# Kernel tuning notes

Measured on AMD Instinct MI355X. Metric: run time of the kernel, lower is better.

Reference implementation:

```python
import jax, jax.numpy as jnp
import numpy as np

EMBED_DIMS = 1024
NUM_HEADS = 16
HEAD_DIMS = EMBED_DIMS // NUM_HEADS


def setup_inputs() -> dict:
    key = jax.random.key(0)
    k_x, k_wqkv, k_bqkv, k_wp, k_bp = jax.random.split(key, 5)
    B, N, D = 2, 2048, EMBED_DIMS
    x = jax.random.normal(k_x, (B, N, D), dtype=jnp.float32)
    # torch nn.Linear(in, out): weight [out, in], y = x @ W.T + b
    s = 1.0 / np.sqrt(D)
    W_qkv = jax.random.uniform(k_wqkv, (3 * D, D), jnp.float32, -s, s)
    b_qkv = jax.random.uniform(k_bqkv, (3 * D,), jnp.float32, -s, s)
    W_proj = jax.random.uniform(k_wp, (D, D), jnp.float32, -s, s)
    b_proj = jax.random.uniform(k_bp, (D,), jnp.float32, -s, s)
    return {"x": x, "W_qkv": W_qkv, "b_qkv": b_qkv, "W_proj": W_proj, "b_proj": b_proj}


def reference(x, W_qkv, b_qkv, W_proj, b_proj):
    B, N, D = x.shape
    H, Hd = NUM_HEADS, HEAD_DIMS
    # qkv projection: [B, N, 3, H, Hd] -> split q, k, v as [B, H, N, Hd]
    qkv = (x @ W_qkv.T + b_qkv).reshape(B, N, 3, H, Hd).transpose(2, 0, 3, 1, 4)
    q, k, v = qkv[0], qkv[1], qkv[2]
    scale = 1.0 / jnp.sqrt(jnp.asarray(Hd, x.dtype))
    attn = jnp.einsum("bhqd,bhkd->bhqk", q, k) * scale  # [B, H, N, N]
    attn = jax.nn.softmax(attn, axis=-1)
    out = jnp.einsum("bhqk,bhkd->bhqd", attn, v)  # [B, H, N, Hd]
    out = out.transpose(0, 2, 1, 3).reshape(B, N, D)
    out = out @ W_proj.T + b_proj
    return out
```

## Files before the change

kernel.cpp:

```cpp
#include <hip/hip_runtime.h>

typedef _Float16 f16x8 __attribute__((ext_vector_type(8)));
typedef __attribute__((ext_vector_type(4))) float f32x4;

static __device__ __forceinline__ unsigned short f2h(float f) {
  return __builtin_bit_cast(unsigned short, (_Float16)f);
}

static __device__ __forceinline__ unsigned int pk2(float a, float b) {
  return (unsigned int)f2h(a) | ((unsigned int)f2h(b) << 16);
}

#if __has_builtin(__builtin_amdgcn_cvt_pkrtz)
static __device__ __forceinline__ unsigned int pkrtz(float a, float b) {
  return __builtin_bit_cast(unsigned int, __builtin_amdgcn_cvt_pkrtz(a, b));
}
#else
#define pkrtz pk2
#endif

#if __has_builtin(__builtin_amdgcn_exp2f)
#define EXP2(x) __builtin_amdgcn_exp2f(x)
#else
#define EXP2(x) exp2f(x)
#endif

#define GLOAD_LDS16(gp, lp)                                          \
  __builtin_amdgcn_global_load_lds(                                  \
      (const __attribute__((address_space(1))) unsigned int*)(gp),   \
      (__attribute__((address_space(3))) unsigned int*)(lp), 16, 0, 0)

__global__ __launch_bounds__(256) void cvt_all(
    const float* __restrict__ X, const float* __restrict__ Wq,
    const float* __restrict__ Wp, unsigned short* __restrict__ Xb,
    unsigned short* __restrict__ Wqb, unsigned short* __restrict__ Wpb) {
  const int i = blockIdx.x * 256 + threadIdx.x;
  const float4* src;
  unsigned short* dst;
  int off;
  if (i < 1048576) {
    src = (const float4*)X; dst = Xb; off = i;
  } else if (i < 1835008) {
    src = (const float4*)Wq; dst = Wqb; off = i - 1048576;
  } else {
    src = (const float4*)Wp; dst = Wpb; off = i - 1835008;
  }
  const float4 v = src[off];
  *(ushort4*)(dst + (size_t)off * 4) =
      make_ushort4(f2h(v.x), f2h(v.y), f2h(v.z), f2h(v.w));
}

__global__ __launch_bounds__(256, 3) void qkv_gemm(
    const unsigned short* __restrict__ Xb, const unsigned short* __restrict__ Wb,
    const float* __restrict__ bias, unsigned short* __restrict__ Qb,
    unsigned short* __restrict__ Kb, unsigned short* __restrict__ Vt) {
  __shared__ __align__(16) unsigned short A_sh[2][128 * 32];
  __shared__ __align__(16) unsigned short B_sh[2][128 * 32];
  const int n0 = blockIdx.x * 128, m0 = blockIdx.y * 128;
  const int tid = threadIdx.x, lane = tid & 63, wave = tid >> 6;
  const int wr = wave >> 1, wc = wave & 1;
  const int lm = lane & 15, lg = lane >> 4;
  const int r4 = lane >> 2;
  const int sg8 = (((lane & 3) ^ ((r4 >> 1) & 3)) * 8);
  const int lgx = (lg ^ ((lm >> 1) & 3)) * 8;

  f32x4 acc[4][4] = {};

#define QSTAGE(k0_, b_)                                                       \
  do {                                                                        \
    _Pragma("unroll")                                                         \
    for (int j = 0; j < 2; ++j) {                                             \
      const int chunk = wave * 2 + j;                                         \
      const int row = chunk * 16 + r4;                                        \
      GLOAD_LDS16(Xb + (size_t)(m0 + row) * 1024 + (k0_) + sg8,               \
                  &A_sh[b_][chunk * 512]);                                    \
      GLOAD_LDS16(Wb + (size_t)(n0 + row) * 1024 + (k0_) + sg8,               \
                  &B_sh[b_][chunk * 512]);                                    \
    }                                                                         \
  } while (0)

  QSTAGE(0, 0);

  for (int it = 0; it < 32; ++it) {
    const int cur = it & 1;
    __syncthreads();
    if (it < 31) QSTAGE((it + 1) * 32, cur ^ 1);

    f16x8 af[4], bfr[4];
#pragma unroll
    for (int mi = 0; mi < 4; ++mi)
      af[mi] = *(const f16x8*)&A_sh[cur][(wr * 64 + mi * 16 + lm) * 32 + lgx];
#pragma unroll
    for (int ni = 0; ni < 4; ++ni)
      bfr[ni] = *(const f16x8*)&B_sh[cur][(wc * 64 + ni * 16 + lm) * 32 + lgx];
    __builtin_amdgcn_s_setprio(1);
#pragma unroll
    for (int mi = 0; mi < 4; ++mi)
#pragma unroll
      for (int ni = 0; ni < 4; ++ni)
        acc[mi][ni] = __builtin_amdgcn_mfma_f32_16x16x32_f16(
            af[mi], bfr[ni], acc[mi][ni], 0, 0, 0);
    __builtin_amdgcn_s_setprio(0);
  }
#undef QSTAGE

  const float qscale = 0.18033688011112042f;
#pragma unroll
  for (int mi = 0; mi < 4; ++mi) {
#pragma unroll
    for (int ni = 0; ni < 4; ++ni) {
      const int gn = n0 + wc * 64 + ni * 16 + lm;
      const float bv = bias[gn];
      const int which = gn >> 10;
      const int h = (gn >> 6) & 15;
      const int hd = gn & 63;
      float v[4];
#pragma unroll
      for (int r = 0; r < 4; ++r) v[r] = acc[mi][ni][r] + bv;
      const int gm0 = m0 + wr * 64 + mi * 16 + lg * 4;
      const int bb = gm0 >> 11;
      const int nq0 = gm0 & 2047;
      if (which == 0) {
        unsigned short* p = Qb + (((size_t)bb * 16 + h) * 2048 + nq0) * 64 + hd;
        p[0] = f2h(v[0] * qscale);   p[64] = f2h(v[1] * qscale);
        p[128] = f2h(v[2] * qscale); p[192] = f2h(v[3] * qscale);
      } else if (which == 1) {
        unsigned short* p = Kb + (((size_t)bb * 16 + h) * 2048 + nq0) * 64 + hd;
        p[0] = f2h(v[0]);   p[64] = f2h(v[1]);
        p[128] = f2h(v[2]); p[192] = f2h(v[3]);
      } else {
        *(ushort4*)(Vt + (((size_t)bb * 16 + h) * 64 + hd) * 2048 + nq0) =
            make_ushort4(f2h(v[0]), f2h(v[1]), f2h(v[2]), f2h(v[3]));
      }
    }
  }
}

__global__ __launch_bounds__(1024, 4) void attn_kernel(
    const unsigned short* __restrict__ Qb, const unsigned short* __restrict__ Kb,
    const unsigned short* __restrict__ Vt, unsigned short* __restrict__ Ob) {
  __shared__ __align__(16) unsigned short K_sh[2][2][64 * 32];
  __shared__ __align__(16) unsigned short V_sh[2][2][64 * 32];
  __shared__ __align__(16) f32x4 Om[8][5][64];
  const int bh = blockIdx.y, q0 = blockIdx.x * 256;
  const size_t base = (size_t)bh * (2048 * 64);
  const unsigned short* Qp = Qb + base;
  const unsigned short* Kp = Kb + base;
  const unsigned short* Vp = Vt + base;
  const int tid = threadIdx.x, lane = tid & 63, wave = tid >> 6;
  const int lm = lane & 15, lg = lane >> 4;
  const int r4 = lane >> 2;
  const int sg8 = (((lane & 3) ^ ((r4 >> 1) & 3)) * 8);
  const int lgx = (lg ^ ((lm >> 1) & 3)) * 8;

  const int qg = wave >> 1;
  const int khalf = wave & 1;

  f16x8 vones;
#pragma unroll
  for (int j = 0; j < 8; ++j) vones[j] = (_Float16)1.0f;

  f16x8 qf[2][2];
#pragma unroll
  for (int mi = 0; mi < 2; ++mi)
#pragma unroll
    for (int kc = 0; kc < 2; ++kc)
      qf[mi][kc] = *(const f16x8*)(Qp +
          (size_t)(q0 + qg * 32 + mi * 16 + lm) * 64 + kc * 32 + lg * 8);

  f32x4 o[2][4] = {};
  f32x4 o_ones[2] = {};

  const bool isV = wave >= 8;
  const int sw = wave & 7;
  const int plane = sw & 1;
  const int chunk = sw >> 1;

#define STAGE(kt_, b_)                                                        \
  do {                                                                        \
    if (!isV) {                                                               \
      GLOAD_LDS16(Kp + (size_t)((kt_) * 64 + chunk * 16 + r4) * 64 +          \
                      plane * 32 + sg8,                                       \
                  &K_sh[b_][plane][chunk * 512]);                             \
    } else {                                                                  \
      GLOAD_LDS16(Vp + (size_t)(chunk * 16 + r4) * 2048 +                     \
                      (kt_) * 64 + plane * 32 + sg8,                          \
                  &V_sh[b_][plane][chunk * 512]);                             \
    }                                                                         \
  } while (0)

  STAGE(0, 0);

  for (int kt = 0; kt < 32; ++kt) {
    const int cur = kt & 1;
    __syncthreads();
    if (kt < 31) STAGE(kt + 1, cur ^ 1);

    f32x4 s[2][2] = {};
#pragma unroll
    for (int kc = 0; kc < 2; ++kc) {
#pragma unroll
      for (int ni = 0; ni < 2; ++ni) {
        const f16x8 kf = *(const f16x8*)
            &K_sh[cur][kc][(khalf * 32 + ni * 16 + lm) * 32 + lgx];
        __builtin_amdgcn_s_setprio(1);
        s[0][ni] = __builtin_amdgcn_mfma_f32_16x16x32_f16(
            kf, qf[0][kc], s[0][ni], 0, 0, 0);
        s[1][ni] = __builtin_amdgcn_mfma_f32_16x16x32_f16(
            kf, qf[1][kc], s[1][ni], 0, 0, 0);
        __builtin_amdgcn_s_setprio(0);
      }
    }

    unsigned int Wp_[2][2][2];
#pragma unroll
    for (int mi = 0; mi < 2; ++mi)
#pragma unroll
      for (int ni = 0; ni < 2; ++ni) {
        const float p0 = EXP2(s[mi][ni][0]), p1 = EXP2(s[mi][ni][1]);
        const float p2 = EXP2(s[mi][ni][2]), p3 = EXP2(s[mi][ni][3]);
        Wp_[mi][ni][0] = pkrtz(p0, p1);
        Wp_[mi][ni][1] = pkrtz(p2, p3);
      }

    f16x8 vb[4];
#pragma unroll
    for (int ni = 0; ni < 4; ++ni)
      vb[ni] = *(const f16x8*)&V_sh[cur][khalf][(ni * 16 + lm) * 32 + lgx];

#pragma unroll
    for (int mi = 0; mi < 2; ++mi) {
      auto t0 = __builtin_amdgcn_permlane32_swap(Wp_[mi][0][0], Wp_[mi][1][0],
                                                 false, false);
      auto u0 = __builtin_amdgcn_permlane16_swap(t0[0], t0[1], false, false);
      auto t1 = __builtin_amdgcn_permlane32_swap(Wp_[mi][0][1], Wp_[mi][1][1],
                                                 false, false);
      auto u1 = __builtin_amdgcn_permlane16_swap(t1[0], t1[1], false, false);
      union { unsigned int u[4]; f16x8 v; } pa;
      pa.u[0] = u0[0];
      pa.u[1] = u1[0];
      pa.u[2] = u0[1];
      pa.u[3] = u1[1];
      __builtin_amdgcn_s_setprio(1);
#pragma unroll
      for (int ni = 0; ni < 4; ++ni)
        o[mi][ni] = __builtin_amdgcn_mfma_f32_16x16x32_f16(
            pa.v, vb[ni], o[mi][ni], 0, 0, 0);
      o_ones[mi] = __builtin_amdgcn_mfma_f32_16x16x32_f16(
          pa.v, vones, o_ones[mi], 0, 0, 0);
      __builtin_amdgcn_s_setprio(0);
    }
  }
#undef STAGE

  const int b = bh >> 4, h = bh & 15;
#pragma unroll
  for (int mi = 0; mi < 2; ++mi) {
    __syncthreads();
    if (khalf == 1) {
#pragma unroll
      for (int ni = 0; ni < 4; ++ni) Om[qg][ni][lane] = o[mi][ni];
      Om[qg][4][lane] = o_ones[mi];
    }
    __syncthreads();
    if (khalf == 0) {
#pragma unroll
      for (int ni = 0; ni < 4; ++ni) {
        const f32x4 t = Om[qg][ni][lane];
        o[mi][ni][0] += t[0]; o[mi][ni][1] += t[1];
        o[mi][ni][2] += t[2]; o[mi][ni][3] += t[3];
      }
      const f32x4 t4 = Om[qg][4][lane];
#pragma unroll
      for (int r = 0; r < 4; ++r) {
        const float inv = 1.0f / (o_ones[mi][r] + t4[r]);
        const int nq = q0 + qg * 32 + mi * 16 + lg * 4 + r;
        unsigned short* p = Ob + ((size_t)(b * 2048 + nq) * 16 + h) * 64 + lm;
        p[0] = f2h(o[mi][0][r] * inv);
        p[16] = f2h(o[mi][1][r] * inv);
        p[32] = f2h(o[mi][2][r] * inv);
        p[48] = f2h(o[mi][3][r] * inv);
      }
    }
  }
}

__global__ __launch_bounds__(256) void proj_gemm(
    const unsigned short* __restrict__ A, const unsigned short* __restrict__ Wb,
    const float* __restrict__ bias, float* __restrict__ Out) {
  __shared__ __align__(16) unsigned short A_sh[2][64 * 32];
  __shared__ __align__(16) unsigned short B_sh[2][128 * 32];
  const int n0 = blockIdx.x * 128, m0 = blockIdx.y * 64;
  const int tid = threadIdx.x, lane = tid & 63, wave = tid >> 6;
  const int wr = wave >> 1, wc = wave & 1, lm = lane & 15, lg = lane >> 4;
  const int r4 = lane >> 2;
  const int sg8 = (((lane & 3) ^ ((r4 >> 1) & 3)) * 8);
  const int lgx = (lg ^ ((lm >> 1) & 3)) * 8;

  f32x4 acc[2][4] = {};

#define PSTAGE(k0_, b_)                                                       \
  do {                                                                        \
    {                                                                         \
      const int row = wave * 16 + r4;                                         \
      GLOAD_LDS16(A + (size_t)(m0 + row) * 1024 + (k0_) + sg8,                \
                  &A_sh[b_][wave * 512]);                                     \
    }                                                                         \
    _Pragma("unroll")                                                         \
    for (int j = 0; j < 2; ++j) {                                             \
      const int chunk = wave * 2 + j;                                         \
      const int row = chunk * 16 + r4;                                        \
      GLOAD_LDS16(Wb + (size_t)(n0 + row) * 1024 + (k0_) + sg8,               \
                  &B_sh[b_][chunk * 512]);                                    \
    }                                                                         \
  } while (0)

  PSTAGE(0, 0);

  for (int it = 0; it < 32; ++it) {
    const int cur = it & 1;
    __syncthreads();
    if (it < 31) PSTAGE((it + 1) * 32, cur ^ 1);

    f16x8 af[2], bfr[4];
#pragma unroll
    for (int mi = 0; mi < 2; ++mi)
      af[mi] = *(const f16x8*)&A_sh[cur][(wr * 32 + mi * 16 + lm) * 32 + lgx];
#pragma unroll
    for (int ni = 0; ni < 4; ++ni)
      bfr[ni] = *(const f16x8*)&B_sh[cur][(wc * 64 + ni * 16 + lm) * 32 + lgx];
#pragma unroll
    for (int mi = 0; mi < 2; ++mi)
#pragma unroll
      for (int ni = 0; ni < 4; ++ni)
        acc[mi][ni] = __builtin_amdgcn_mfma_f32_16x16x32_f16(
            af[mi], bfr[ni], acc[mi][ni], 0, 0, 0);
  }
#undef PSTAGE

#pragma unroll
  for (int mi = 0; mi < 2; ++mi)
#pragma unroll
    for (int ni = 0; ni < 4; ++ni) {
      const int gn = n0 + wc * 64 + ni * 16 + lm;
      const float bv = bias[gn];
#pragma unroll
      for (int r = 0; r < 4; ++r) {
        const int gm = m0 + wr * 32 + mi * 16 + lg * 4 + r;
        Out[(size_t)gm * 1024 + gn] = acc[mi][ni][r] + bv;
      }
    }
}

extern "C" void kernel_launch(void* const* d_in, const int* in_sizes, int n_in,
                              void* d_out, int out_size, void* d_ws, size_t ws_size,
                              hipStream_t stream) {
  const float* x      = (const float*)d_in[0];
  const float* W_qkv  = (const float*)d_in[1];
  const float* b_qkv  = (const float*)d_in[2];
  const float* W_proj = (const float*)d_in[3];
  const float* b_proj = (const float*)d_in[4];
  float* out = (float*)d_out;

  unsigned short* Qb  = (unsigned short*)d_ws;
  unsigned short* Kb  = Qb + 4194304;
  unsigned short* Vt  = Kb + 4194304;
  unsigned short* Ao  = Vt + 4194304;
  unsigned short* Xb  = Ao + 4194304;
  unsigned short* Wqb = Xb + 4194304;
  unsigned short* Wpb = Wqb + 3145728;

  cvt_all<<<8192, 256, 0, stream>>>(x, W_qkv, W_proj, Xb, Wqb, Wpb);
  qkv_gemm<<<dim3(24, 32), 256, 0, stream>>>(Xb, Wqb, b_qkv, Qb, Kb, Vt);
  attn_kernel<<<dim3(8, 32), 1024, 0, stream>>>(Qb, Kb, Vt, Ao);
  proj_gemm<<<dim3(8, 64), 256, 0, stream>>>(Ao, Wpb, b_proj, out);
}
```

Measured before the change: 182.1 us.

## Stage two KV tiles per barrier in attention and raise GEMM occupancy bounds

The attention kernel now loads two 64-key tiles per pipeline stage into doubled LDS buffers, so there is one __syncthreads per 128 keys instead of per 64. The QK MFMA priority bump now wraps the whole score loop rather than each pair. The qkv and proj GEMMs also get a min-blocks-per-CU of 4 in launch_bounds, which pushes register use down. In exchange, attention LDS use roughly doubles for K/V, which may lower occupancy, and the tighter register limits on the GEMMs could cause spills.

After: 179.2 us. Within noise of the previous version (-1.6%).

```diff
diff --git a/kernel.cpp b/kernel.cpp
--- a/kernel.cpp
+++ b/kernel.cpp
@@ -50,7 +50,7 @@
       make_ushort4(f2h(v.x), f2h(v.y), f2h(v.z), f2h(v.w));
 }
 
-__global__ __launch_bounds__(256, 3) void qkv_gemm(
+__global__ __launch_bounds__(256, 4) void qkv_gemm(
     const unsigned short* __restrict__ Xb, const unsigned short* __restrict__ Wb,
     const float* __restrict__ bias, unsigned short* __restrict__ Qb,
     unsigned short* __restrict__ Kb, unsigned short* __restrict__ Vt) {
@@ -139,8 +139,8 @@
 __global__ __launch_bounds__(1024, 4) void attn_kernel(
     const unsigned short* __restrict__ Qb, const unsigned short* __restrict__ Kb,
     const unsigned short* __restrict__ Vt, unsigned short* __restrict__ Ob) {
-  __shared__ __align__(16) unsigned short K_sh[2][2][64 * 32];
-  __shared__ __align__(16) unsigned short V_sh[2][2][64 * 32];
+  __shared__ __align__(16) unsigned short K_sh[2][2][2][64 * 32];
+  __shared__ __align__(16) unsigned short V_sh[2][2][2][64 * 32];
   __shared__ __align__(16) f32x4 Om[8][5][64];
   const int bh = blockIdx.y, q0 = blockIdx.x * 256;
   const size_t base = (size_t)bh * (2048 * 64);
@@ -176,82 +176,91 @@
   const int plane = sw & 1;
   const int chunk = sw >> 1;
 
-#define STAGE(kt_, b_)                                                        \
+#define STAGE1(kt_, b_, t_)                                                   \
   do {                                                                        \
     if (!isV) {                                                               \
       GLOAD_LDS16(Kp + (size_t)((kt_) * 64 + chunk * 16 + r4) * 64 +          \
                       plane * 32 + sg8,                                       \
-                  &K_sh[b_][plane][chunk * 512]);                             \
+                  &K_sh[b_][t_][plane][chunk * 512]);                         \
     } else {                                                                  \
       GLOAD_LDS16(Vp + (size_t)(chunk * 16 + r4) * 2048 +                     \
                       (kt_) * 64 + plane * 32 + sg8,                          \
-                  &V_sh[b_][plane][chunk * 512]);                             \
+                  &V_sh[b_][t_][plane][chunk * 512]);                         \
     }                                                                         \
   } while (0)
 
-  STAGE(0, 0);
-
-  for (int kt = 0; kt < 32; ++kt) {
-    const int cur = kt & 1;
-    __syncthreads();
-    if (kt < 31) STAGE(kt + 1, cur ^ 1);
-
-    f32x4 s[2][2] = {};
-#pragma unroll
-    for (int kc = 0; kc < 2; ++kc) {
-#pragma unroll
-      for (int ni = 0; ni < 2; ++ni) {
-        const f16x8 kf = *(const f16x8*)
-            &K_sh[cur][kc][(khalf * 32 + ni * 16 + lm) * 32 + lgx];
-        __builtin_amdgcn_s_setprio(1);
-        s[0][ni] = __builtin_amdgcn_mfma_f32_16x16x32_f16(
-            kf, qf[0][kc], s[0][ni], 0, 0, 0);
-        s[1][ni] = __builtin_amdgcn_mfma_f32_16x16x32_f16(
-            kf, qf[1][kc], s[1][ni], 0, 0, 0);
-        __builtin_amdgcn_s_setprio(0);
-      }
-    }
-
-    unsigned int Wp_[2][2][2];
-#pragma unroll
-    for (int mi = 0; mi < 2; ++mi)
-#pragma unroll
-      for (int ni = 0; ni < 2; ++ni) {
-        const float p0 = EXP2(s[mi][ni][0]), p1 = EXP2(s[mi][ni][1]);
-        const float p2 = EXP2(s[mi][ni][2]), p3 = EXP2(s[mi][ni][3]);
-        Wp_[mi][ni][0] = pkrtz(p0, p1);
-        Wp_[mi][ni][1] = pkrtz(p2, p3);
-      }
-
-    f16x8 vb[4];
-#pragma unroll
-    for (int ni = 0; ni < 4; ++ni)
-      vb[ni] = *(const f16x8*)&V_sh[cur][khalf][(ni * 16 + lm) * 32 + lgx];
-
-#pragma unroll
-    for (int mi = 0; mi < 2; ++mi) {
-      auto t0 = __builtin_amdgcn_permlane32_swap(Wp_[mi][0][0], Wp_[mi][1][0],
-                                                 false, false);
-      auto u0 = __builtin_amdgcn_permlane16_swap(t0[0], t0[1], false, false);
-      auto t1 = __builtin_amdgcn_permlane32_swap(Wp_[mi][0][1], Wp_[mi][1][1],
-                                                 false, false);
-      auto u1 = __builtin_amdgcn_permlane16_swap(t1[0], t1[1], false, false);
-      union { unsigned int u[4]; f16x8 v; } pa;
-      pa.u[0] = u0[0];
-      pa.u[1] = u1[0];
-      pa.u[2] = u0[1];
-      pa.u[3] = u1[1];
-      __builtin_amdgcn_s_setprio(1);
-#pragma unroll
-      for (int ni = 0; ni < 4; ++ni)
-        o[mi][ni] = __builtin_amdgcn_mfma_f32_16x16x32_f16(
-            pa.v, vb[ni], o[mi][ni], 0, 0, 0);
-      o_ones[mi] = __builtin_amdgcn_mfma_f32_16x16x32_f16(
-          pa.v, vones, o_ones[mi], 0, 0, 0);
-      __builtin_amdgcn_s_setprio(0);
-    }
-  }
-#undef STAGE
+#define STAGE2(seg_, b_)                                                      \
+  do { STAGE1(2 * (seg_), b_, 0); STAGE1(2 * (seg_) + 1, b_, 1); } while (0)
+
+#define TILE_COMPUTE(cur_, t_)                                                \
+  do {                                                                        \
+    f32x4 s[2][2] = {};                                                       \
+    __builtin_amdgcn_s_setprio(1);                                            \
+    _Pragma("unroll")                                                         \
+    for (int kc = 0; kc < 2; ++kc) {                                          \
+      _Pragma("unroll")                                                       \
+      for (int ni = 0; ni < 2; ++ni) {                                        \
+        const f16x8 kf = *(const f16x8*)                                      \
+            &K_sh[cur_][t_][kc][(khalf * 32 + ni * 16 + lm) * 32 + lgx];      \
+        s[0][ni] = __builtin_amdgcn_mfma_f32_16x16x32_f16(                    \
+            kf, qf[0][kc], s[0][ni], 0, 0, 0);                                \
+        s[1][ni] = __builtin_amdgcn_mfma_f32_16x16x32_f16(                    \
+            kf, qf[1][kc], s[1][ni], 0, 0, 0);                                \
+      }                                                                       \
+    }                                                                         \
+    __builtin_amdgcn_s_setprio(0);                                            \
+    unsigned int Wp_[2][2][2];                                                \
+    _Pragma("unroll")                                                         \
+    for (int mi = 0; mi < 2; ++mi) {                                          \
+      _Pragma("unroll")                                                       \
+      for (int ni = 0; ni < 2; ++ni) {                                        \
+        const float p0 = EXP2(s[mi][ni][0]), p1 = EXP2(s[mi][ni][1]);         \
+        const float p2 = EXP2(s[mi][ni][2]), p3 = EXP2(s[mi][ni][3]);         \
+        Wp_[mi][ni][0] = pkrtz(p0, p1);                                       \
+        Wp_[mi][ni][1] = pkrtz(p2, p3);                                       \
+      }                                                                       \
+    }                                                                         \
+    f16x8 vb[4];                                                              \
+    _Pragma("unroll")                                                         \
+    for (int ni = 0; ni < 4; ++ni)                                            \
+      vb[ni] = *(const f16x8*)                                                \
+          &V_sh[cur_][t_][khalf][(ni * 16 + lm) * 32 + lgx];                  \
+    _Pragma("unroll")                                                         \
+    for (int mi = 0; mi < 2; ++mi) {                                          \
+      auto t0 = __builtin_amdgcn_permlane32_swap(Wp_[mi][0][0], Wp_[mi][1][0],\
+                                                 false, false);               \
+      auto u0 = __builtin_amdgcn_permlane16_swap(t0[0], t0[1], false, false); \
+      auto t1 = __builtin_amdgcn_permlane32_swap(Wp_[mi][0][1], Wp_[mi][1][1],\
+                                                 false, false);               \
+      auto u1 = __builtin_amdgcn_permlane16_swap(t1[0], t1[1], false, false); \
+      union { unsigned int u[4]; f16x8 v; } pa;                               \
+      pa.u[0] = u0[0];                                                        \
+      pa.u[1] = u1[0];                                                        \
+      pa.u[2] = u0[1];                                                        \
+      pa.u[3] = u1[1];                                                        \
+      __builtin_amdgcn_s_setprio(1);                                          \
+      _Pragma("unroll")                                                       \
+      for (int ni = 0; ni < 4; ++ni)                                          \
+        o[mi][ni] = __builtin_amdgcn_mfma_f32_16x16x32_f16(                   \
+            pa.v, vb[ni], o[mi][ni], 0, 0, 0);                                \
+      o_ones[mi] = __builtin_amdgcn_mfma_f32_16x16x32_f16(                    \
+          pa.v, vones, o_ones[mi], 0, 0, 0);                                  \
+      __builtin_amdgcn_s_setprio(0);                                          \
+    }                                                                         \
+  } while (0)
+
+  STAGE2(0, 0);
+
+  for (int seg = 0; seg < 16; ++seg) {
+    const int cur = seg & 1;
+    __syncthreads();
+    if (seg < 15) STAGE2(seg + 1, cur ^ 1);
+    TILE_COMPUTE(cur, 0);
+    TILE_COMPUTE(cur, 1);
+  }
+#undef STAGE1
+#undef STAGE2
+#undef TILE_COMPUTE
 
   const int b = bh >> 4, h = bh & 15;
 #pragma unroll
@@ -285,7 +294,7 @@
   }
 }
 
-__global__ __launch_bounds__(256) void proj_gemm(
+__global__ __launch_bounds__(256, 4) void proj_gemm(
     const unsigned short* __restrict__ A, const unsigned short* __restrict__ Wb,
     const float* __restrict__ bias, float* __restrict__ Out) {
   __shared__ __align__(16) unsigned short A_sh[2][64 * 32];
```
